# Kernel optimization log

Hardware: AMD Instinct MI355X
Metric: run time of the kernel (lower is better)

Reference implementation:

```python
import jax, jax.numpy as jnp
import numpy as np

N_EMBED = 256
HEAD_SIZE = 64
B, T = 32, 768

def setup_inputs() -> dict:
    key = jax.random.key(0)
    kx, kq, kk, kv = jax.random.split(key, 4)
    bound = 1.0 / np.sqrt(N_EMBED)  # torch nn.Linear default init
    return {
        "x": jax.random.normal(kx, (B, T, N_EMBED), dtype=jnp.float32),
        "wq": jax.random.uniform(kq, (N_EMBED, HEAD_SIZE), minval=-bound, maxval=bound, dtype=jnp.float32),
        "wk": jax.random.uniform(kk, (N_EMBED, HEAD_SIZE), minval=-bound, maxval=bound, dtype=jnp.float32),
        "wv": jax.random.uniform(kv, (N_EMBED, HEAD_SIZE), minval=-bound, maxval=bound, dtype=jnp.float32),
    }

def reference(x, wq, wk, wv):
    # x: [B, T, C]; wq/wk/wv: [C, H]
    q = jnp.einsum('btc,ch->bth', x, wq)
    k = jnp.einsum('btc,ch->bth', x, wk)
    v = jnp.einsum('btc,ch->bth', x, wv)
    scale = k.shape[-1] ** -0.5
    scores = jnp.einsum('bqh,bkh->bqk', q, k) * scale  # [B, T, T]
    Tn = x.shape[1]
    causal = jnp.tril(jnp.ones((Tn, Tn), dtype=bool))
    scores = jnp.where(causal, scores, -jnp.inf)
    attn = jax.nn.softmax(scores, axis=-1)
    # dropout omitted (eval mode) for deterministic reference
    return jnp.einsum('bqk,bkh->bqh', attn, v)
```

## Files before the change

### kernel.cpp

```cpp
#include <hip/hip_runtime.h>
#include <hip/hip_bf16.h>

#define B_  32
#define T_  768
#define C_  256
#define H_  64
#define BT_ (B_*T_)
#define WT_OFF (3*BT_*H_)

using short8 = __attribute__((ext_vector_type(8))) short;
using f32x4  = __attribute__((ext_vector_type(4))) float;

__device__ __forceinline__ ushort f2bf(float f) {
    union { float f; unsigned u; } v; v.f = f;
    unsigned u = v.u;
    return (ushort)((u + 0x7FFFu + ((u >> 16) & 1u)) >> 16);
}

__global__ __launch_bounds__(256) void prep_w_kernel(
    const float* __restrict__ wq, const float* __restrict__ wk,
    const float* __restrict__ wv, ushort* __restrict__ ws)
{
    const int idx = blockIdx.x*256 + threadIdx.x;
    const int m = idx >> 14, r = idx & 16383;
    const int h = r >> 8, k = r & 255;
    const float* w = (m == 0) ? wq : (m == 1) ? wk : wv;
    ws[WT_OFF + idx] = f2bf(w[k*H_ + h]);
}

__global__ __launch_bounds__(256) void qkv_proj_kernel(
    const float* __restrict__ x, ushort* __restrict__ ws)
{
    __shared__ ushort wT[64][264];
    __shared__ ushort vls[64][72];
    const int tid   = threadIdx.x;
    const int wv_id = tid >> 6;
    const int lane  = tid & 63;
    const int g     = lane >> 4;
    const int c     = lane & 15;
    const int rowbase = blockIdx.x*64;
    const int row     = rowbase + wv_id*16 + c;
    const int sh = tid >> 2, ss = tid & 3;

    short8 a[8];
    const float* xr = x + row*C_;
    #pragma unroll
    for (int ch = 0; ch < 8; ++ch) {
        const float4 f0 = *(const float4*)(xr + ch*32 + g*8);
        const float4 f1 = *(const float4*)(xr + ch*32 + g*8 + 4);
        short8 t;
        t[0]=(short)f2bf(f0.x); t[1]=(short)f2bf(f0.y); t[2]=(short)f2bf(f0.z); t[3]=(short)f2bf(f0.w);
        t[4]=(short)f2bf(f1.x); t[5]=(short)f2bf(f1.y); t[6]=(short)f2bf(f1.z); t[7]=(short)f2bf(f1.w);
        a[ch] = t;
    }

    const ushort* wtg = ws + WT_OFF;
    #pragma unroll
    for (int i = 0; i < 8; ++i)
        *(short8*)&wT[sh][ss*64 + i*8] = *(const short8*)(wtg + sh*256 + ss*64 + i*8);
    __syncthreads();

    for (int m = 0; m < 3; ++m) {
        #pragma unroll
        for (int jn = 0; jn < 4; ++jn) {
            f32x4 acc = {0.f, 0.f, 0.f, 0.f};
            #pragma unroll
            for (int ch = 0; ch < 8; ++ch) {
                const short8 bw = *(const short8*)(&wT[jn*16 + c][ch*32 + g*8]);
                acc = __builtin_amdgcn_mfma_f32_16x16x32_bf16(a[ch], bw, acc, 0, 0, 0);
            }
            if (m < 2) {
                #pragma unroll
                for (int r = 0; r < 4; ++r)
                    vls[wv_id*16 + g*4 + r][jn*16 + c] = f2bf(acc[r]);
            } else {
                #pragma unroll
                for (int r = 0; r < 4; ++r)
                    vls[jn*16 + c][wv_id*16 + g*4 + r] = f2bf(acc[r]);
            }
        }
        __syncthreads();
        {
            ushort* dst = (m < 2)
                ? (ws + m*BT_*H_ + (rowbase + sh)*H_ + ss*16)
                : (ws + 2*BT_*H_ + sh*BT_ + rowbase + ss*16);
            *(short8*)(dst)     = *(const short8*)&vls[sh][ss*16];
            *(short8*)(dst + 8) = *(const short8*)&vls[sh][ss*16 + 8];
            if (m < 2) {
                const ushort* src = wtg + (m+1)*16384 + sh*256 + ss*64;
                #pragma unroll
                for (int i = 0; i < 8; ++i)
                    *(short8*)&wT[sh][ss*64 + i*8] = *(const short8*)(src + i*8);
            }
        }
        __syncthreads();
    }
}

__global__ __launch_bounds__(256) void attn_kernel(
    const ushort* __restrict__ ws, float* __restrict__ out)
{
    __shared__ ushort kls[2][64][72];
    __shared__ ushort vls[2][64][72];
    __shared__ ushort pls[4][16][72];

    const int tid   = threadIdx.x;
    const int wv_id = tid >> 6;
    const int lane  = tid & 63;
    const int g     = lane >> 4;
    const int c     = lane & 15;
    const int qt    = 11 - (blockIdx.x >> 5);
    const int b     = blockIdx.x & 31;
    const int nkt   = qt + 1;
    const int sh = tid >> 2, ss = tid & 3;

    const ushort* kg  = ws + BT_*H_ + b*T_*H_;
    const ushort* vtg = ws + 2*BT_*H_ + b*T_;

    short8 aq[2];
    const ushort* qp = ws + (b*T_ + qt*64 + wv_id*16 + c)*H_;
    aq[0] = *(const short8*)(qp + g*8);
    aq[1] = *(const short8*)(qp + 32 + g*8);

    float m_[4], l_[4];
    f32x4 o[4];
    #pragma unroll
    for (int r = 0; r < 4; ++r) { m_[r] = -INFINITY; l_[r] = 0.f; }
    #pragma unroll
    for (int jh = 0; jh < 4; ++jh) o[jh] = (f32x4){0.f, 0.f, 0.f, 0.f};

    short8 kreg0, kreg1, vreg0, vreg1;
    #define LOAD_TILES(kt_) do { \
        const ushort* ksrc = kg + ((kt_)*64 + sh)*H_ + ss*16;       \
        kreg0 = *(const short8*)ksrc; kreg1 = *(const short8*)(ksrc + 8); \
        const ushort* vsrc = vtg + sh*BT_ + (kt_)*64 + ss*16;       \
        vreg0 = *(const short8*)vsrc; vreg1 = *(const short8*)(vsrc + 8); \
    } while (0)
    #define WRITE_TILES(bi_) do { \
        *(short8*)&kls[bi_][sh][ss*16]     = kreg0; \
        *(short8*)&kls[bi_][sh][ss*16 + 8] = kreg1; \
        *(short8*)&vls[bi_][sh][ss*16]     = vreg0; \
        *(short8*)&vls[bi_][sh][ss*16 + 8] = vreg1; \
    } while (0)

    LOAD_TILES(0);
    WRITE_TILES(0);
    __syncthreads();

    int cur = 0;
    for (int kt = 0; kt < nkt; ++kt) {
        const bool more = (kt + 1 < nkt);
        if (more) LOAD_TILES(kt + 1);

        f32x4 s[4];
        #pragma unroll
        for (int j = 0; j < 4; ++j) {
            f32x4 acc = {0.f, 0.f, 0.f, 0.f};
            #pragma unroll
            for (int ch = 0; ch < 2; ++ch) {
                const short8 bk = *(const short8*)(&kls[cur][j*16 + c][ch*32 + g*8]);
                acc = __builtin_amdgcn_mfma_f32_16x16x32_bf16(aq[ch], bk, acc, 0, 0, 0);
            }
            s[j] = acc;
        }

        const bool diag = (kt == qt);
        #pragma unroll
        for (int j = 0; j < 4; ++j) {
            #pragma unroll
            for (int r = 0; r < 4; ++r) {
                float v = s[j][r] * 0.125f;
                if (diag && (j*16 + c > wv_id*16 + g*4 + r)) v = -1e30f;
                s[j][r] = v;
            }
        }

        #pragma unroll
        for (int r = 0; r < 4; ++r) {
            float tm = fmaxf(fmaxf(s[0][r], s[1][r]), fmaxf(s[2][r], s[3][r]));
            tm = fmaxf(tm, __shfl_xor(tm, 1));
            tm = fmaxf(tm, __shfl_xor(tm, 2));
            tm = fmaxf(tm, __shfl_xor(tm, 4));
            tm = fmaxf(tm, __shfl_xor(tm, 8));
            const float mn = fmaxf(m_[r], tm);
            const float al = __expf(m_[r] - mn);
            m_[r] = mn;
            float ps = 0.f;
            #pragma unroll
            for (int j = 0; j < 4; ++j) {
                const float p = __expf(s[j][r] - mn);
                s[j][r] = p;
                ps += p;
            }
            ps += __shfl_xor(ps, 1);
            ps += __shfl_xor(ps, 2);
            ps += __shfl_xor(ps, 4);
            ps += __shfl_xor(ps, 8);
            l_[r] = l_[r]*al + ps;
            #pragma unroll
            for (int jh = 0; jh < 4; ++jh) o[jh][r] *= al;
        }

        #pragma unroll
        for (int j = 0; j < 4; ++j) {
            #pragma unroll
            for (int r = 0; r < 4; ++r)
                pls[wv_id][g*4 + r][j*16 + c] = f2bf(s[j][r]);
        }

        #pragma unroll
        for (int c2 = 0; c2 < 2; ++c2) {
            const short8 ap = *(const short8*)(&pls[wv_id][c][c2*32 + g*8]);
            #pragma unroll
            for (int jh = 0; jh < 4; ++jh) {
                const short8 bv = *(const short8*)(&vls[cur][jh*16 + c][c2*32 + g*8]);
                o[jh] = __builtin_amdgcn_mfma_f32_16x16x32_bf16(ap, bv, o[jh], 0, 0, 0);
            }
        }

        if (more) WRITE_TILES(cur ^ 1);
        __syncthreads();
        cur ^= 1;
    }

    float* op = out + (b*T_ + qt*64 + wv_id*16)*H_;
    #pragma unroll
    for (int r = 0; r < 4; ++r) {
        const float inv = 1.0f / l_[r];
        #pragma unroll
        for (int jh = 0; jh < 4; ++jh)
            op[(g*4 + r)*H_ + jh*16 + c] = o[jh][r] * inv;
    }
    #undef LOAD_TILES
    #undef WRITE_TILES
}

extern "C" void kernel_launch(void* const* d_in, const int* in_sizes, int n_in,
                              void* d_out, int out_size, void* d_ws, size_t ws_size,
                              hipStream_t stream) {
    const float* x  = (const float*)d_in[0];
    const float* wq = (const float*)d_in[1];
    const float* wk = (const float*)d_in[2];
    const float* wv = (const float*)d_in[3];
    ushort* ws = (ushort*)d_ws;

    prep_w_kernel<<<dim3(192), dim3(256), 0, stream>>>(wq, wk, wv, ws);
    qkv_proj_kernel<<<dim3(BT_/64), dim3(256), 0, stream>>>(x, ws);
    attn_kernel<<<dim3(B_*12), dim3(256), 0, stream>>>(ws, (float*)d_out);
}
```

Measured before the change: 108.9 us.

## Transpose QK^T MFMA so each lane owns one query row; fold scale into Q

Swaps the MFMA operands for the score product so each lane holds all keys of one query row. The online-softmax max and sum then need only two cross-lane shuffles per tile instead of sixteen, and each lane keeps one running max and sum instead of four. The 1/sqrt(d) scale is folded into Q at projection time, and P is written to LDS as packed 64-bit stores. It adds a per-row shuffle to broadcast the rescale factor and the final sum into the output layout, and rounding Q to bf16 after the 0.125 scale changes the numerics slightly.

```diff
diff --git a/kernel.cpp b/kernel.cpp
--- a/kernel.cpp
+++ b/kernel.cpp
@@ -69,7 +69,11 @@
                 const short8 bw = *(const short8*)(&wT[jn*16 + c][ch*32 + g*8]);
                 acc = __builtin_amdgcn_mfma_f32_16x16x32_bf16(a[ch], bw, acc, 0, 0, 0);
             }
-            if (m < 2) {
+            if (m == 0) {
+                #pragma unroll
+                for (int r = 0; r < 4; ++r)
+                    vls[wv_id*16 + g*4 + r][jn*16 + c] = f2bf(acc[r] * 0.125f);
+            } else if (m == 1) {
                 #pragma unroll
                 for (int r = 0; r < 4; ++r)
                     vls[wv_id*16 + g*4 + r][jn*16 + c] = f2bf(acc[r]);
@@ -122,10 +126,8 @@
     aq[0] = *(const short8*)(qp + g*8);
     aq[1] = *(const short8*)(qp + 32 + g*8);
 
-    float m_[4], l_[4];
+    float m_ = -INFINITY, l_ = 0.f;
     f32x4 o[4];
-    #pragma unroll
-    for (int r = 0; r < 4; ++r) { m_[r] = -INFINITY; l_[r] = 0.f; }
     #pragma unroll
     for (int jh = 0; jh < 4; ++jh) o[jh] = (f32x4){0.f, 0.f, 0.f, 0.f};
 
@@ -159,53 +161,55 @@
             #pragma unroll
             for (int ch = 0; ch < 2; ++ch) {
                 const short8 bk = *(const short8*)(&kls[cur][j*16 + c][ch*32 + g*8]);
-                acc = __builtin_amdgcn_mfma_f32_16x16x32_bf16(aq[ch], bk, acc, 0, 0, 0);
+                acc = __builtin_amdgcn_mfma_f32_16x16x32_bf16(bk, aq[ch], acc, 0, 0, 0);
             }
             s[j] = acc;
         }
 
-        const bool diag = (kt == qt);
-        #pragma unroll
-        for (int j = 0; j < 4; ++j) {
+        if (kt == qt) {
+            const int qloc = wv_id*16 + c;
+            #pragma unroll
+            for (int j = 0; j < 4; ++j)
+                #pragma unroll
+                for (int r = 0; r < 4; ++r)
+                    if (j*16 + g*4 + r > qloc) s[j][r] = -1e30f;
+        }
+
+        float tm = s[0][0];
+        #pragma unroll
+        for (int j = 0; j < 4; ++j)
+            #pragma unroll
+            for (int r = 0; r < 4; ++r) tm = fmaxf(tm, s[j][r]);
+        tm = fmaxf(tm, __shfl_xor(tm, 16));
+        tm = fmaxf(tm, __shfl_xor(tm, 32));
+        const float mn = fmaxf(m_, tm);
+        const float al = __expf(m_ - mn);
+        m_ = mn;
+        float ps = 0.f;
+        #pragma unroll
+        for (int j = 0; j < 4; ++j)
             #pragma unroll
             for (int r = 0; r < 4; ++r) {
-                float v = s[j][r] * 0.125f;
-                if (diag && (j*16 + c > wv_id*16 + g*4 + r)) v = -1e30f;
-                s[j][r] = v;
-            }
-        }
-
-        #pragma unroll
-        for (int r = 0; r < 4; ++r) {
-            float tm = fmaxf(fmaxf(s[0][r], s[1][r]), fmaxf(s[2][r], s[3][r]));
-            tm = fmaxf(tm, __shfl_xor(tm, 1));
-            tm = fmaxf(tm, __shfl_xor(tm, 2));
-            tm = fmaxf(tm, __shfl_xor(tm, 4));
-            tm = fmaxf(tm, __shfl_xor(tm, 8));
-            const float mn = fmaxf(m_[r], tm);
-            const float al = __expf(m_[r] - mn);
-            m_[r] = mn;
-            float ps = 0.f;
-            #pragma unroll
-            for (int j = 0; j < 4; ++j) {
                 const float p = __expf(s[j][r] - mn);
                 s[j][r] = p;
                 ps += p;
             }
-            ps += __shfl_xor(ps, 1);
-            ps += __shfl_xor(ps, 2);
-            ps += __shfl_xor(ps, 4);
-            ps += __shfl_xor(ps, 8);
-            l_[r] = l_[r]*al + ps;
-            #pragma unroll
-            for (int jh = 0; jh < 4; ++jh) o[jh][r] *= al;
+        ps += __shfl_xor(ps, 16);
+        ps += __shfl_xor(ps, 32);
+        l_ = l_*al + ps;
+
+        #pragma unroll
+        for (int r = 0; r < 4; ++r) {
+            const float alr = __shfl(al, g*4 + r);
+            #pragma unroll
+            for (int jh = 0; jh < 4; ++jh) o[jh][r] *= alr;
         }
 
         #pragma unroll
         for (int j = 0; j < 4; ++j) {
-            #pragma unroll
-            for (int r = 0; r < 4; ++r)
-                pls[wv_id][g*4 + r][j*16 + c] = f2bf(s[j][r]);
+            const uint lo = (uint)f2bf(s[j][0]) | ((uint)f2bf(s[j][1]) << 16);
+            const uint hi = (uint)f2bf(s[j][2]) | ((uint)f2bf(s[j][3]) << 16);
+            *(uint2*)&pls[wv_id][c][j*16 + g*4] = make_uint2(lo, hi);
         }
 
         #pragma unroll
@@ -226,7 +230,8 @@
     float* op = out + (b*T_ + qt*64 + wv_id*16)*H_;
     #pragma unroll
     for (int r = 0; r < 4; ++r) {
-        const float inv = 1.0f / l_[r];
+        const float lr  = __shfl(l_, g*4 + r);
+        const float inv = 1.0f / lr;
         #pragma unroll
         for (int jh = 0; jh < 4; ++jh)
             op[(g*4 + r)*H_ + jh*16 + c] = o[jh][r] * inv;
```

Result: faster. 103.8 us (-4.7%).
